# Performance work log

Measured on AMD Instinct MI355X. Metric: run time of the kernel, lower is better.

## Reference

```python
import jax, jax.numpy as jnp
import numpy as np

DIM = 1024
NUM_HEADS = 16
SCALE = DIM ** (-0.5)  # NOTE: source scales by full dim, not head_dim


def setup_inputs() -> dict:
    key = jax.random.key(0)
    ks = jax.random.split(key, 10)
    B, N, C = 2, 2048, DIM
    s = 0.02
    return {
        "x": jax.random.normal(ks[0], (B, N, C), dtype=jnp.float32),
        "queries": jax.random.normal(ks[1], (B, N, C), dtype=jnp.float32),
        "wq": jax.random.normal(ks[2], (C, C), dtype=jnp.float32) * s,
        "bq": jnp.zeros((C,), dtype=jnp.float32),
        "wk": jax.random.normal(ks[3], (C, C), dtype=jnp.float32) * s,
        "bk": jnp.zeros((C,), dtype=jnp.float32),
        "wv": jax.random.normal(ks[4], (C, C), dtype=jnp.float32) * s,
        "bv": jnp.zeros((C,), dtype=jnp.float32),
        "wo": jax.random.normal(ks[5], (C, C), dtype=jnp.float32) * s,
        "bo": jnp.zeros((C,), dtype=jnp.float32),
    }


def reference(x, queries, wq, bq, wk, bk, wv, bv, wo, bo):
    B, N, C = queries.shape
    H = NUM_HEADS
    D = C // H
    # torch Linear: y = x @ W.T + b  (W is [out, in])
    q = (queries @ wq.T + bq).reshape(B, N, H, D).transpose(0, 2, 1, 3)  # [B,H,N,D]
    k = (x @ wk.T + bk).reshape(B, N, H, D).transpose(0, 2, 1, 3)
    v = (x @ wv.T + bv).reshape(B, N, H, D).transpose(0, 2, 1, 3)
    attn = jnp.einsum("bhqd,bhkd->bhqk", q, k) * SCALE  # full-dim scale per source
    attn = jax.nn.softmax(attn, axis=-1)
    out = jnp.einsum("bhqk,bhkd->bhqd", attn, v)  # [B,H,N,D]
    out = out.transpose(0, 2, 1, 3).reshape(B, N, C)
    return out @ wo.T + bo
```

## Files before the change

### kernel.cpp

```cpp
#include <hip/hip_runtime.h>

typedef __attribute__((ext_vector_type(8))) short bf16x8;
typedef __attribute__((ext_vector_type(4))) float f32x4;
typedef unsigned short u16;

#define MFMA16(a,b,c) __builtin_amdgcn_mfma_f32_16x16x32_bf16((a),(b),(c),0,0,0)

#if defined(__has_builtin) && __has_builtin(__builtin_amdgcn_exp2f)
#define EXP2(x) __builtin_amdgcn_exp2f(x)
#else
#define EXP2(x) exp2f(x)
#endif

__device__ __forceinline__ u16 f2bf(float f) {
  union { float f; unsigned int u; } v; v.f = f;
  unsigned int r = v.u + 0x7FFFu + ((v.u >> 16) & 1u);
  return (u16)(r >> 16);
}

__device__ __forceinline__ void gld16(const void* g, void* l) {
  __builtin_amdgcn_global_load_lds(
      (__attribute__((address_space(1))) void*)(g),
      (__attribute__((address_space(3))) void*)(l), 16, 0, 0);
}

__global__ __launch_bounds__(256) void cast_all(
    const float* __restrict__ x, const float* __restrict__ qu,
    const float* __restrict__ wq, const float* __restrict__ wk,
    const float* __restrict__ wv, const float* __restrict__ wo,
    u16* __restrict__ xb, u16* __restrict__ qub,
    u16* __restrict__ wqb, u16* __restrict__ wkb,
    u16* __restrict__ wvb, u16* __restrict__ wob)
{
  int i = blockIdx.x * 256 + threadIdx.x;
  const float4* src; u16* dst; int off;
  if (i < 1048576)      { src = (const float4*)qu; dst = qub; off = i; }
  else if (i < 2097152) { src = (const float4*)x;  dst = xb;  off = i - 1048576; }
  else if (i < 2359296) { src = (const float4*)wq; dst = wqb; off = i - 2097152; }
  else if (i < 2621440) { src = (const float4*)wk; dst = wkb; off = i - 2359296; }
  else if (i < 2883584) { src = (const float4*)wv; dst = wvb; off = i - 2621440; }
  else                  { src = (const float4*)wo; dst = wob; off = i - 2883584; }
  float4 v = src[off];
  ushort4 r; r.x = f2bf(v.x); r.y = f2bf(v.y); r.z = f2bf(v.z); r.w = f2bf(v.w);
  ((ushort4*)dst)[off] = r;
}

__global__ __launch_bounds__(256) void gemm_qkv(
    const u16* __restrict__ qub, const u16* __restrict__ xb,
    const u16* __restrict__ wqb, const u16* __restrict__ wkb, const u16* __restrict__ wvb,
    const float* __restrict__ bq, const float* __restrict__ bk, const float* __restrict__ bv,
    u16* __restrict__ qhd, u16* __restrict__ khd, u16* __restrict__ vtd)
{
  __shared__ u16 As[128 * 64];
  __shared__ u16 Bs[128 * 64];
  int tid = threadIdx.x, w = tid >> 6, lane = tid & 63;
  int bm = blockIdx.x, bn = blockIdx.y, z = blockIdx.z;
  int wm = w >> 1, wn = w & 1;
  const u16* A = (z == 0) ? qub : xb;
  const u16* W = (z == 0) ? wqb : (z == 1) ? wkb : wvb;
  f32x4 acc[4][4] = {};
  for (int k0 = 0; k0 < 1024; k0 += 64) {
#pragma unroll
    for (int i = 0; i < 4; i++) {
      int seg = i * 256 + w * 64 + lane;
      int row = seg >> 3, pseg = seg & 7;
      int lseg = pseg ^ (row & 7);
      gld16(A + (size_t)(bm * 128 + row) * 1024 + k0 + lseg * 8,
            &As[(i * 256 + w * 64) * 8]);
      gld16(W + (size_t)(bn * 128 + row) * 1024 + k0 + lseg * 8,
            &Bs[(i * 256 + w * 64) * 8]);
    }
    __syncthreads();
#pragma unroll
    for (int ks = 0; ks < 2; ks++) {
      bf16x8 af[4], bfr[4];
#pragma unroll
      for (int mt = 0; mt < 4; mt++) {
        int row = wm * 64 + mt * 16 + (lane & 15);
        int cseg = (ks * 4 + (lane >> 4)) ^ (row & 7);
        af[mt] = *(const bf16x8*)&As[(row * 8 + cseg) * 8];
      }
#pragma unroll
      for (int nt = 0; nt < 4; nt++) {
        int row = wn * 64 + nt * 16 + (lane & 15);
        int cseg = (ks * 4 + (lane >> 4)) ^ (row & 7);
        bfr[nt] = *(const bf16x8*)&Bs[(row * 8 + cseg) * 8];
      }
#pragma unroll
      for (int mt = 0; mt < 4; mt++)
#pragma unroll
        for (int nt = 0; nt < 4; nt++)
          acc[mt][nt] = MFMA16(af[mt], bfr[nt], acc[mt][nt]);
    }
    __syncthreads();
  }
  const float* bias = (z == 0) ? bq : (z == 1) ? bk : bv;
  u16* dst = (z == 0) ? qhd : khd;
#pragma unroll
  for (int nt = 0; nt < 4; nt++) {
    int o = bn * 128 + wn * 64 + nt * 16 + (lane & 15);
    float bval = bias[o];
    int h = o >> 6, d = o & 63;
#pragma unroll
    for (int mt = 0; mt < 4; mt++)
#pragma unroll
      for (int j = 0; j < 4; j++) {
        int m = bm * 128 + wm * 64 + mt * 16 + (lane >> 4) * 4 + j;
        int b = m >> 11, n = m & 2047;
        float val = acc[mt][nt][j] + bval;
        if (z < 2)
          dst[((size_t)(b * 16 + h) * 2048 + n) * 64 + d] = f2bf(val);
        else
          vtd[((size_t)(b * 16 + h) * 64 + d) * 2048 + n] = f2bf(val);
      }
  }
}

__global__ __launch_bounds__(256) void attn(
    const u16* __restrict__ qh, const u16* __restrict__ kh,
    const u16* __restrict__ vt, u16* __restrict__ ot)
{
  __shared__ u16 Ks[64 * 64];
  __shared__ u16 Vs[64 * 64];
  __shared__ u16 Ps[4][16 * 72];
  int tid = threadIdx.x, w = tid >> 6, lane = tid & 63;
  int qt = blockIdx.x, bh = blockIdx.y;
  const u16* qp = qh + (size_t)bh * 2048 * 64;
  const u16* kp = kh + (size_t)bh * 2048 * 64;
  const u16* vp = vt + (size_t)bh * 64 * 2048;
  int qrow0 = qt * 64 + w * 16;
  bf16x8 aq[2];
#pragma unroll
  for (int ks = 0; ks < 2; ks++)
    aq[ks] = *(const bf16x8*)(qp + (size_t)(qrow0 + (lane & 15)) * 64 + ks * 32 + (lane >> 4) * 8);
  f32x4 O[4] = {};
  float lsum[4] = {0.f, 0.f, 0.f, 0.f};
  const float cexp = 0.0450842298f;
  u16* pw = &Ps[w][0];
  for (int kt = 0; kt < 32; kt++) {
#pragma unroll
    for (int i = 0; i < 2; i++) {
      int seg = (i * 4 + w) * 64 + lane;
      int row = seg >> 3, pseg = seg & 7;
      int lseg = pseg ^ (row & 7);
      gld16(kp + (size_t)(kt * 64 + row) * 64 + lseg * 8, &Ks[((i * 4 + w) * 64) * 8]);
      gld16(vp + (size_t)row * 2048 + kt * 64 + lseg * 8, &Vs[((i * 4 + w) * 64) * 8]);
    }
    __syncthreads();
    f32x4 S[4] = {};
#pragma unroll
    for (int ks = 0; ks < 2; ks++)
#pragma unroll
      for (int nt = 0; nt < 4; nt++) {
        int row = nt * 16 + (lane & 15);
        int cseg = (ks * 4 + (lane >> 4)) ^ (row & 7);
        bf16x8 bfr = *(const bf16x8*)&Ks[(row * 8 + cseg) * 8];
        S[nt] = MFMA16(aq[ks], bfr, S[nt]);
      }
#pragma unroll
    for (int nt = 0; nt < 4; nt++)
#pragma unroll
      for (int j = 0; j < 4; j++) {
        float p = EXP2(S[nt][j] * cexp);
        lsum[j] += p;
        pw[((lane >> 4) * 4 + j) * 72 + nt * 16 + (lane & 15)] = f2bf(p);
      }
#pragma unroll
    for (int ks2 = 0; ks2 < 2; ks2++) {
      bf16x8 af = *(const bf16x8*)&pw[(lane & 15) * 72 + ks2 * 32 + (lane >> 4) * 8];
#pragma unroll
      for (int dt = 0; dt < 4; dt++) {
        int row = dt * 16 + (lane & 15);
        int cseg = (ks2 * 4 + (lane >> 4)) ^ (row & 7);
        bf16x8 bfr = *(const bf16x8*)&Vs[(row * 8 + cseg) * 8];
        O[dt] = MFMA16(af, bfr, O[dt]);
      }
    }
    __syncthreads();
  }
  int b = bh >> 4, h = bh & 15;
  float inv[4];
#pragma unroll
  for (int j = 0; j < 4; j++) {
    float s = lsum[j];
    s += __shfl_xor(s, 1);
    s += __shfl_xor(s, 2);
    s += __shfl_xor(s, 4);
    s += __shfl_xor(s, 8);
    inv[j] = 1.0f / s;
  }
#pragma unroll
  for (int dt = 0; dt < 4; dt++)
#pragma unroll
    for (int j = 0; j < 4; j++) {
      int n = qt * 64 + w * 16 + (lane >> 4) * 4 + j;
      ot[((size_t)(b * 2048 + n) * 16 + h) * 64 + dt * 16 + (lane & 15)] =
          f2bf(O[dt][j] * inv[j]);
    }
}

__global__ __launch_bounds__(256) void gemm_out(
    const u16* __restrict__ Aot, const u16* __restrict__ wob,
    const float* __restrict__ bo, float* __restrict__ out)
{
  __shared__ u16 As[128 * 64];
  __shared__ u16 Bs[128 * 64];
  int tid = threadIdx.x, w = tid >> 6, lane = tid & 63;
  int bm = blockIdx.x, bn = blockIdx.y;
  int wm = w >> 1, wn = w & 1;
  f32x4 acc[4][4] = {};
  for (int k0 = 0; k0 < 1024; k0 += 64) {
#pragma unroll
    for (int i = 0; i < 4; i++) {
      int seg = i * 256 + w * 64 + lane;
      int row = seg >> 3, pseg = seg & 7;
      int lseg = pseg ^ (row & 7);
      gld16(Aot + (size_t)(bm * 128 + row) * 1024 + k0 + lseg * 8,
            &As[(i * 256 + w * 64) * 8]);
      gld16(wob + (size_t)(bn * 128 + row) * 1024 + k0 + lseg * 8,
            &Bs[(i * 256 + w * 64) * 8]);
    }
    __syncthreads();
#pragma unroll
    for (int ks = 0; ks < 2; ks++) {
      bf16x8 af[4], bfr[4];
#pragma unroll
      for (int mt = 0; mt < 4; mt++) {
        int row = wm * 64 + mt * 16 + (lane & 15);
        int cseg = (ks * 4 + (lane >> 4)) ^ (row & 7);
        af[mt] = *(const bf16x8*)&As[(row * 8 + cseg) * 8];
      }
#pragma unroll
      for (int nt = 0; nt < 4; nt++) {
        int row = wn * 64 + nt * 16 + (lane & 15);
        int cseg = (ks * 4 + (lane >> 4)) ^ (row & 7);
        bfr[nt] = *(const bf16x8*)&Bs[(row * 8 + cseg) * 8];
      }
#pragma unroll
      for (int mt = 0; mt < 4; mt++)
#pragma unroll
        for (int nt = 0; nt < 4; nt++)
          acc[mt][nt] = MFMA16(af[mt], bfr[nt], acc[mt][nt]);
    }
    __syncthreads();
  }
#pragma unroll
  for (int nt = 0; nt < 4; nt++) {
    int o = bn * 128 + wn * 64 + nt * 16 + (lane & 15);
    float bval = bo[o];
#pragma unroll
    for (int mt = 0; mt < 4; mt++)
#pragma unroll
      for (int j = 0; j < 4; j++) {
        int m = bm * 128 + wm * 64 + mt * 16 + (lane >> 4) * 4 + j;
        out[(size_t)m * 1024 + o] = acc[mt][nt][j] + bval;
      }
  }
}

extern "C" void kernel_launch(void* const* d_in, const int* in_sizes, int n_in,
                              void* d_out, int out_size, void* d_ws, size_t ws_size,
                              hipStream_t stream)
{
  const float* x  = (const float*)d_in[0];
  const float* qu = (const float*)d_in[1];
  const float* wq = (const float*)d_in[2];
  const float* bq = (const float*)d_in[3];
  const float* wk = (const float*)d_in[4];
  const float* bk = (const float*)d_in[5];
  const float* wv = (const float*)d_in[6];
  const float* bv = (const float*)d_in[7];
  const float* wo = (const float*)d_in[8];
  const float* bo = (const float*)d_in[9];
  float* out = (float*)d_out;
  char* ws = (char*)d_ws;
  u16* xb  = (u16*)(ws + (size_t)0);
  u16* qub = (u16*)(ws + ((size_t)8  << 20));
  u16* wqb = (u16*)(ws + ((size_t)16 << 20));
  u16* wkb = (u16*)(ws + ((size_t)18 << 20));
  u16* wvb = (u16*)(ws + ((size_t)20 << 20));
  u16* wob = (u16*)(ws + ((size_t)22 << 20));
  u16* qhd = (u16*)(ws + ((size_t)24 << 20));
  u16* khd = (u16*)(ws + ((size_t)32 << 20));
  u16* vtd = (u16*)(ws + ((size_t)40 << 20));
  u16* otd = (u16*)(ws + ((size_t)48 << 20));

  cast_all<<<12288, 256, 0, stream>>>(x, qu, wq, wk, wv, wo,
                                      xb, qub, wqb, wkb, wvb, wob);
  gemm_qkv<<<dim3(32, 8, 3), 256, 0, stream>>>(qub, xb, wqb, wkb, wvb,
                                               bq, bk, bv, qhd, khd, vtd);
  attn<<<dim3(32, 32), 256, 0, stream>>>(qhd, khd, vtd, otd);
  gemm_out<<<dim3(32, 8), 256, 0, stream>>>(otd, wob, bo, out);
}
```

Before: 241.5 us.

## Restructure attention to split keys across waves and retile output GEMM

The attention kernel is restructured so each wave processes a quarter of the key sequence for all 64 queries. K and V fragments are held in registers loaded directly from global memory, and probabilities are exchanged through shared memory, with partial row sums combined at the end. The softmax scale is folded into Q during the projection epilogue, and V is stored with a permuted column order to match the packed P layout. The output GEMM tile shrinks to 64 rows so twice as many blocks launch, and the attention kernel requests two blocks per CU. Together these aim to cut per-tile synchronisation and LDS staging and to raise occupancy, at the cost of more register pressure and direct global fragment loads.

```diff
diff --git a/kernel.cpp b/kernel.cpp
--- a/kernel.cpp
+++ b/kernel.cpp
@@ -1,8 +1,10 @@
 #include <hip/hip_runtime.h>
+#include <hip/hip_bf16.h>
 
 typedef __attribute__((ext_vector_type(8))) short bf16x8;
 typedef __attribute__((ext_vector_type(4))) float f32x4;
 typedef unsigned short u16;
+typedef unsigned int u32;
 
 #define MFMA16(a,b,c) __builtin_amdgcn_mfma_f32_16x16x32_bf16((a),(b),(c),0,0,0)
 
@@ -12,10 +14,18 @@
 #define EXP2(x) exp2f(x)
 #endif
 
+#define QSCALE 0.045084220027780106f
+
 __device__ __forceinline__ u16 f2bf(float f) {
   union { float f; unsigned int u; } v; v.f = f;
   unsigned int r = v.u + 0x7FFFu + ((v.u >> 16) & 1u);
   return (u16)(r >> 16);
+}
+
+__device__ __forceinline__ u32 pkbf(float a, float b) {
+  union { __hip_bfloat162 h; u32 u; } cv;
+  cv.h = __float22bfloat162_rn(make_float2(a, b));
+  return cv.u;
 }
 
 __device__ __forceinline__ void gld16(const void* g, void* l) {
@@ -108,94 +118,113 @@
         int m = bm * 128 + wm * 64 + mt * 16 + (lane >> 4) * 4 + j;
         int b = m >> 11, n = m & 2047;
         float val = acc[mt][nt][j] + bval;
-        if (z < 2)
+        if (z == 0)
+          dst[((size_t)(b * 16 + h) * 2048 + n) * 64 + d] = f2bf(val * QSCALE);
+        else if (z == 1)
           dst[((size_t)(b * 16 + h) * 2048 + n) * 64 + d] = f2bf(val);
-        else
-          vtd[((size_t)(b * 16 + h) * 64 + d) * 2048 + n] = f2bf(val);
-      }
-  }
-}
-
-__global__ __launch_bounds__(256) void attn(
+        else {
+          int np = (n & ~63) | ((n & 15) << 2) | ((n >> 4) & 3);
+          vtd[((size_t)(b * 16 + h) * 64 + d) * 2048 + np] = f2bf(val);
+        }
+      }
+  }
+}
+
+__global__ __launch_bounds__(256, 2) void attn(
     const u16* __restrict__ qh, const u16* __restrict__ kh,
     const u16* __restrict__ vt, u16* __restrict__ ot)
 {
-  __shared__ u16 Ks[64 * 64];
-  __shared__ u16 Vs[64 * 64];
-  __shared__ u16 Ps[4][16 * 72];
+  __shared__ u16 Pb[4][64 * 72];
+  __shared__ u16 Qs[64 * 72];
+  __shared__ float Ls[4][64];
   int tid = threadIdx.x, w = tid >> 6, lane = tid & 63;
+  int c = lane & 15, quad = lane >> 4;
   int qt = blockIdx.x, bh = blockIdx.y;
-  const u16* qp = qh + (size_t)bh * 2048 * 64;
-  const u16* kp = kh + (size_t)bh * 2048 * 64;
+  const u16* qp = qh + ((size_t)bh * 2048 + qt * 64) * 64;
+  const u16* kp = kh + ((size_t)bh * 2048 + w * 512) * 64;
   const u16* vp = vt + (size_t)bh * 64 * 2048;
-  int qrow0 = qt * 64 + w * 16;
-  bf16x8 aq[2];
-#pragma unroll
-  for (int ks = 0; ks < 2; ks++)
-    aq[ks] = *(const bf16x8*)(qp + (size_t)(qrow0 + (lane & 15)) * 64 + ks * 32 + (lane >> 4) * 8);
+
+  {
+    int row = tid >> 2, ch = tid & 3;
+    *(bf16x8*)&Qs[row * 72 + ch * 16]     = *(const bf16x8*)(qp + row * 64 + ch * 16);
+    *(bf16x8*)&Qs[row * 72 + ch * 16 + 8] = *(const bf16x8*)(qp + row * 64 + ch * 16 + 8);
+  }
+  bf16x8 Kf[4][2];
+#pragma unroll
+  for (int nt = 0; nt < 4; nt++)
+#pragma unroll
+    for (int ks = 0; ks < 2; ks++)
+      Kf[nt][ks] = *(const bf16x8*)(kp + (size_t)(nt * 16 + c) * 64 + ks * 32 + quad * 8);
+  __syncthreads();
+
   f32x4 O[4] = {};
-  float lsum[4] = {0.f, 0.f, 0.f, 0.f};
-  const float cexp = 0.0450842298f;
-  u16* pw = &Ps[w][0];
-  for (int kt = 0; kt < 32; kt++) {
-#pragma unroll
-    for (int i = 0; i < 2; i++) {
-      int seg = (i * 4 + w) * 64 + lane;
-      int row = seg >> 3, pseg = seg & 7;
-      int lseg = pseg ^ (row & 7);
-      gld16(kp + (size_t)(kt * 64 + row) * 64 + lseg * 8, &Ks[((i * 4 + w) * 64) * 8]);
-      gld16(vp + (size_t)row * 2048 + kt * 64 + lseg * 8, &Vs[((i * 4 + w) * 64) * 8]);
-    }
-    __syncthreads();
-    f32x4 S[4] = {};
-#pragma unroll
-    for (int ks = 0; ks < 2; ks++)
-#pragma unroll
-      for (int nt = 0; nt < 4; nt++) {
-        int row = nt * 16 + (lane & 15);
-        int cseg = (ks * 4 + (lane >> 4)) ^ (row & 7);
-        bf16x8 bfr = *(const bf16x8*)&Ks[(row * 8 + cseg) * 8];
-        S[nt] = MFMA16(aq[ks], bfr, S[nt]);
-      }
-#pragma unroll
-    for (int nt = 0; nt < 4; nt++)
+  f32x4 ls[4] = {};
+  bf16x8 Vf[4][2];
+  for (int it = 0; it < 8; it++) {
+#pragma unroll
+    for (int b = 0; b < 4; b++)
+#pragma unroll
+      for (int ks2 = 0; ks2 < 2; ks2++)
+        Vf[b][ks2] = *(const bf16x8*)(vp + (size_t)(w * 16 + c) * 2048 +
+                                      (b * 8 + it) * 64 + ks2 * 32 + quad * 8);
+#pragma unroll
+    for (int mt = 0; mt < 4; mt++) {
+      bf16x8 q0 = *(const bf16x8*)&Qs[(mt * 16 + c) * 72 + quad * 8];
+      bf16x8 q1 = *(const bf16x8*)&Qs[(mt * 16 + c) * 72 + 32 + quad * 8];
+      f32x4 S0 = {}, S1 = {}, S2 = {}, S3 = {};
+      S0 = MFMA16(q0, Kf[0][0], S0); S0 = MFMA16(q1, Kf[0][1], S0);
+      S1 = MFMA16(q0, Kf[1][0], S1); S1 = MFMA16(q1, Kf[1][1], S1);
+      S2 = MFMA16(q0, Kf[2][0], S2); S2 = MFMA16(q1, Kf[2][1], S2);
+      S3 = MFMA16(q0, Kf[3][0], S3); S3 = MFMA16(q1, Kf[3][1], S3);
 #pragma unroll
       for (int j = 0; j < 4; j++) {
-        float p = EXP2(S[nt][j] * cexp);
-        lsum[j] += p;
-        pw[((lane >> 4) * 4 + j) * 72 + nt * 16 + (lane & 15)] = f2bf(p);
-      }
-#pragma unroll
-    for (int ks2 = 0; ks2 < 2; ks2++) {
-      bf16x8 af = *(const bf16x8*)&pw[(lane & 15) * 72 + ks2 * 32 + (lane >> 4) * 8];
-#pragma unroll
-      for (int dt = 0; dt < 4; dt++) {
-        int row = dt * 16 + (lane & 15);
-        int cseg = (ks2 * 4 + (lane >> 4)) ^ (row & 7);
-        bf16x8 bfr = *(const bf16x8*)&Vs[(row * 8 + cseg) * 8];
-        O[dt] = MFMA16(af, bfr, O[dt]);
-      }
-    }
-    __syncthreads();
-  }
-  int b = bh >> 4, h = bh & 15;
-  float inv[4];
-#pragma unroll
-  for (int j = 0; j < 4; j++) {
-    float s = lsum[j];
-    s += __shfl_xor(s, 1);
-    s += __shfl_xor(s, 2);
-    s += __shfl_xor(s, 4);
-    s += __shfl_xor(s, 8);
-    inv[j] = 1.0f / s;
-  }
-#pragma unroll
-  for (int dt = 0; dt < 4; dt++)
+        float p0 = EXP2(S0[j]), p1 = EXP2(S1[j]);
+        float p2 = EXP2(S2[j]), p3 = EXP2(S3[j]);
+        ls[mt][j] += (p0 + p1) + (p2 + p3);
+        uint2 pk; pk.x = pkbf(p0, p1); pk.y = pkbf(p2, p3);
+        *(uint2*)&Pb[w][(mt * 16 + quad * 4 + j) * 72 + c * 4] = pk;
+      }
+    }
+    if (it < 7) {
+#pragma unroll
+      for (int nt = 0; nt < 4; nt++)
+#pragma unroll
+        for (int ks = 0; ks < 2; ks++)
+          Kf[nt][ks] = *(const bf16x8*)(kp + (size_t)((it + 1) * 64 + nt * 16 + c) * 64 +
+                                        ks * 32 + quad * 8);
+    }
+    __syncthreads();
+#pragma unroll
+    for (int b = 0; b < 4; b++)
+#pragma unroll
+      for (int ks2 = 0; ks2 < 2; ks2++) {
+#pragma unroll
+        for (int mt = 0; mt < 4; mt++) {
+          bf16x8 pa = *(const bf16x8*)&Pb[b][(mt * 16 + c) * 72 + ks2 * 32 + quad * 8];
+          O[mt] = MFMA16(pa, Vf[b][ks2], O[mt]);
+        }
+      }
+    __syncthreads();
+  }
+#pragma unroll
+  for (int mt = 0; mt < 4; mt++)
 #pragma unroll
     for (int j = 0; j < 4; j++) {
-      int n = qt * 64 + w * 16 + (lane >> 4) * 4 + j;
-      ot[((size_t)(b * 2048 + n) * 16 + h) * 64 + dt * 16 + (lane & 15)] =
-          f2bf(O[dt][j] * inv[j]);
+      float s = ls[mt][j];
+      s += __shfl_xor(s, 1); s += __shfl_xor(s, 2);
+      s += __shfl_xor(s, 4); s += __shfl_xor(s, 8);
+      if (c == 0) Ls[w][mt * 16 + quad * 4 + j] = s;
+    }
+  __syncthreads();
+  int b_ = bh >> 4, h = bh & 15;
+#pragma unroll
+  for (int mt = 0; mt < 4; mt++)
+#pragma unroll
+    for (int j = 0; j < 4; j++) {
+      int q = mt * 16 + quad * 4 + j;
+      float inv = 1.0f / (Ls[0][q] + Ls[1][q] + Ls[2][q] + Ls[3][q]);
+      int n = qt * 64 + q;
+      ot[(((size_t)b_ * 2048 + n) * 16 + h) * 64 + w * 16 + c] = f2bf(O[mt][j] * inv);
     }
 }
 
@@ -203,30 +232,36 @@
     const u16* __restrict__ Aot, const u16* __restrict__ wob,
     const float* __restrict__ bo, float* __restrict__ out)
 {
-  __shared__ u16 As[128 * 64];
+  __shared__ u16 As[64 * 64];
   __shared__ u16 Bs[128 * 64];
   int tid = threadIdx.x, w = tid >> 6, lane = tid & 63;
   int bm = blockIdx.x, bn = blockIdx.y;
   int wm = w >> 1, wn = w & 1;
-  f32x4 acc[4][4] = {};
+  f32x4 acc[2][4] = {};
   for (int k0 = 0; k0 < 1024; k0 += 64) {
 #pragma unroll
-    for (int i = 0; i < 4; i++) {
-      int seg = i * 256 + w * 64 + lane;
+    for (int i = 0; i < 2; i++) {
+      int seg = i * 256 + tid;
       int row = seg >> 3, pseg = seg & 7;
       int lseg = pseg ^ (row & 7);
-      gld16(Aot + (size_t)(bm * 128 + row) * 1024 + k0 + lseg * 8,
-            &As[(i * 256 + w * 64) * 8]);
+      gld16(Aot + (size_t)(bm * 64 + row) * 1024 + k0 + lseg * 8,
+            &As[(i * 256 + tid - (tid & 7)) * 8 + (tid & 7) * 8]);
+    }
+#pragma unroll
+    for (int i = 0; i < 4; i++) {
+      int seg = i * 256 + tid;
+      int row = seg >> 3, pseg = seg & 7;
+      int lseg = pseg ^ (row & 7);
       gld16(wob + (size_t)(bn * 128 + row) * 1024 + k0 + lseg * 8,
-            &Bs[(i * 256 + w * 64) * 8]);
+            &Bs[(i * 256 + tid - (tid & 7)) * 8 + (tid & 7) * 8]);
     }
     __syncthreads();
 #pragma unroll
     for (int ks = 0; ks < 2; ks++) {
-      bf16x8 af[4], bfr[4];
-#pragma unroll
-      for (int mt = 0; mt < 4; mt++) {
-        int row = wm * 64 + mt * 16 + (lane & 15);
+      bf16x8 af[2], bfr[4];
+#pragma unroll
+      for (int mt = 0; mt < 2; mt++) {
+        int row = wm * 32 + mt * 16 + (lane & 15);
         int cseg = (ks * 4 + (lane >> 4)) ^ (row & 7);
         af[mt] = *(const bf16x8*)&As[(row * 8 + cseg) * 8];
       }
@@ -237,7 +272,7 @@
         bfr[nt] = *(const bf16x8*)&Bs[(row * 8 + cseg) * 8];
       }
 #pragma unroll
-      for (int mt = 0; mt < 4; mt++)
+      for (int mt = 0; mt < 2; mt++)
 #pragma unroll
         for (int nt = 0; nt < 4; nt++)
           acc[mt][nt] = MFMA16(af[mt], bfr[nt], acc[mt][nt]);
@@ -249,10 +284,10 @@
     int o = bn * 128 + wn * 64 + nt * 16 + (lane & 15);
     float bval = bo[o];
 #pragma unroll
-    for (int mt = 0; mt < 4; mt++)
+    for (int mt = 0; mt < 2; mt++)
 #pragma unroll
       for (int j = 0; j < 4; j++) {
-        int m = bm * 128 + wm * 64 + mt * 16 + (lane >> 4) * 4 + j;
+        int m = bm * 64 + wm * 32 + mt * 16 + (lane >> 4) * 4 + j;
         out[(size_t)m * 1024 + o] = acc[mt][nt][j] + bval;
       }
   }
@@ -290,5 +325,5 @@
   gemm_qkv<<<dim3(32, 8, 3), 256, 0, stream>>>(qub, xb, wqb, wkb, wvb,
                                                bq, bk, bv, qhd, khd, vtd);
   attn<<<dim3(32, 32), 256, 0, stream>>>(qhd, khd, vtd, otd);
-  gemm_out<<<dim3(32, 8), 256, 0, stream>>>(otd, wob, bo, out);
-}
+  gemm_out<<<dim3(64, 8), 256, 0, stream>>>(otd, wob, bo, out);
+}
```

Measured after the change: 239.9 us. About the same (-0.7%).
